# Performance work log

Hardware: AMD Instinct MI355X
Metric: run time of the kernel (lower is better)

The kernel has to match this reference:

```python
import jax, jax.numpy as jnp
import numpy as np

B, T, D, N, K, H = 2, 2048, 2048, 16, 8, 128
WIN = 1024                      # sliding_window_size
SOFT_CAP = 50.0                 # attn_logits_soft_cap
SCALAR = 0.08838834764831845    # query_pre_attn_scalar = head_dim**-0.5
K_MASK = -2.3819763e+38
ROPE_BASE = 10000.0
ROPE_SCALE = 1.0


def apply_rope(x, positions):
    # x: [B, T, heads, H]; positions: [B, T]
    head_dim = x.shape[-1]
    half = head_dim // 2
    timescale = ROPE_BASE ** (2.0 * jnp.arange(half, dtype=jnp.float32) / head_dim)
    sinusoid = positions[..., None].astype(jnp.float32) / timescale / ROPE_SCALE  # [B,T,half]
    sin = jnp.sin(sinusoid)[:, :, None, :]
    cos = jnp.cos(sinusoid)[:, :, None, :]
    first, second = jnp.split(x, 2, axis=-1)
    return jnp.concatenate(
        [first * cos - second * sin, second * cos + first * sin], axis=-1
    ).astype(x.dtype)


def setup_inputs() -> dict:
    key = jax.random.key(0)
    k0, k1, k2, k3 = jax.random.split(key, 4)
    x = jax.random.normal(k0, (B, T, D), jnp.float32)
    wq = jax.random.normal(k1, (N, D, H), jnp.float32) * (D ** -0.5)
    wkv = jax.random.normal(k2, (2, K, D, H), jnp.float32) * (D ** -0.5)
    wo = jax.random.normal(k3, (N, H, D), jnp.float32) * ((N * H) ** -0.5)
    segment_pos = jnp.broadcast_to(jnp.arange(T, dtype=jnp.int32), (B, T))
    attn_mask = jnp.broadcast_to(jnp.tril(jnp.ones((T, T), dtype=bool)), (B, T, T))  # causal
    return {"x": x, "wq": wq, "wkv": wkv, "wo": wo,
            "segment_pos": segment_pos, "attn_mask": attn_mask}


def reference(x, wq, wkv, wo, segment_pos, attn_mask):
    # --- projections ---
    q = jnp.einsum('BTD,NDH->BTNH', x, wq)          # [B,T,N,H]
    kv = jnp.einsum('BTD,CKDH->CBTKH', x, wkv)      # [2,B,T,K,H]
    k_proj, v_proj = kv[0], kv[1]
    # --- RoPE + query scaling ---
    q = apply_rope(q, segment_pos) * SCALAR
    k_proj = apply_rope(k_proj, segment_pos)
    # --- GQA logits ---
    G = N // K
    qg = q.reshape(B, T, K, G, H)
    logits = jnp.einsum('BTKGH,BSKH->BTKGS', qg, k_proj).reshape(B, T, N, T)
    # --- soft cap ---
    logits = jnp.tanh(logits / SOFT_CAP) * SOFT_CAP
    # --- sliding-window mask combined with causal attn_mask ---
    all_ones = jnp.ones(attn_mask.shape, dtype=attn_mask.dtype)
    sliding_mask = jnp.triu(all_ones, -WIN + 1) * jnp.tril(all_ones, WIN - 1)
    mask = sliding_mask * attn_mask                  # [B,T,S]
    padded_logits = jnp.where(mask[:, :, None, :], logits, K_MASK)
    probs = jax.nn.softmax(padded_logits, axis=-1).astype(k_proj.dtype)
    # --- GQA weighted values ---
    encoded = jnp.einsum('BTKGS,BSKH->BTKGH',
                         probs.reshape(B, T, K, G, T), v_proj).reshape(B, T, N, H)
    # --- output projection ---
    return jnp.einsum('BTNH,NHD->BTD', encoded, wo)
```

## Files before the change

### kernel.cpp

```cpp
#include <hip/hip_runtime.h>
#include <hip/hip_bf16.h>
#include <stdint.h>

#define BDIM 2
#define TDIM 2048
#define DDIM 2048
#define NHEADS 16
#define KVH 8
#define HDIM 128
#define WINSZ 1024
#define BT (BDIM*TDIM)
#define NHD (NHEADS*HDIM)
#define QKVC 4096

typedef unsigned short u16;
typedef __attribute__((ext_vector_type(8))) short bf16x8;
typedef __attribute__((ext_vector_type(4))) float f32x4;

__device__ __forceinline__ u16 f2bf(float f) {
  union { float f; unsigned u; } v; v.f = f;
  unsigned r = v.u + 0x7FFFu + ((v.u >> 16) & 1u);
  return (u16)(r >> 16);
}
__device__ __forceinline__ float bf2f(u16 u) {
  union { unsigned u; float f; } v; v.u = ((unsigned)u) << 16;
  return v.f;
}
__device__ __forceinline__ u16 cvt_bf(float f) {
  __hip_bfloat16 hb = __float2bfloat16(f);
  return *reinterpret_cast<u16*>(&hb);
}

__device__ __forceinline__ void gl_lds16(const u16* g, u16* l) {
  __builtin_amdgcn_global_load_lds((const __attribute__((address_space(1))) void*)g,
                                   (__attribute__((address_space(3))) void*)l, 16, 0, 0);
}

__global__ __launch_bounds__(256) void k_prep(const float* __restrict__ x, const float* __restrict__ wq,
                                              const float* __restrict__ wkv, const float* __restrict__ wo,
                                              const int* __restrict__ seg,
                                              u16* __restrict__ x_bf, u16* __restrict__ wt_qkv,
                                              u16* __restrict__ wo_t, float2* __restrict__ tab) {
  const int id = blockIdx.x, tid = threadIdx.x;
  if (id < 8192) {
    __shared__ float tl0[32][33];
    int tx = tid & 31, ty = tid >> 5;
    int r0 = (id & 127) * 32, c0 = (id >> 7) * 32;
    #pragma unroll
    for (int i = 0; i < 4; i++) {
      int r = r0 + tx, c = c0 + ty + i*8;
      const float* sp; size_t off;
      if (r < 2048) { sp = wq; off = (size_t)(r >> 7)*262144u + (size_t)(r & 127); }
      else { int j = r - 2048; sp = wkv; off = (size_t)((j >> 10)*8 + ((j >> 7) & 7))*262144u + (size_t)(j & 127); }
      off += (size_t)c * 128u;
      tl0[tx][ty + i*8] = sp[off];
    }
    __syncthreads();
    #pragma unroll
    for (int i = 0; i < 4; i++) {
      int rl = ty + i*8;
      wt_qkv[(size_t)(r0 + rl)*2048u + (size_t)(c0 + tx)] = f2bf(tl0[rl][tx]);
    }
  } else if (id < 16384) {
    int i = (id - 8192)*256 + tid;
    float4 v = ((const float4*)x)[i];
    ushort4 o;
    o.x = f2bf(v.x); o.y = f2bf(v.y); o.z = f2bf(v.z); o.w = f2bf(v.w);
    ((ushort4*)x_bf)[i] = o;
  } else if (id < 20480) {
    __shared__ float tl1[32][33];
    int id3 = id - 16384;
    int tx = tid & 31, ty = tid >> 5;
    int r0 = (id3 & 63) * 32, c0 = (id3 >> 6) * 32;
    #pragma unroll
    for (int i = 0; i < 4; i++) {
      int r = r0 + tx, c = c0 + ty + i*8;
      tl1[tx][ty + i*8] = wo[(size_t)c * 2048u + (size_t)r];
    }
    __syncthreads();
    #pragma unroll
    for (int i = 0; i < 4; i++) {
      int rl = ty + i*8;
      wo_t[(size_t)(r0 + rl)*2048u + (size_t)(c0 + tx)] = f2bf(tl1[rl][tx]);
    }
  } else {
    int bt = (id - 20480)*4 + (tid >> 6);
    int i = tid & 63;
    int pos = seg[bt];
    float inv_ts = exp2f(-(float)i * (13.287712379549449f/64.0f));
    float ang = (float)pos * inv_ts;
    tab[(size_t)bt*64 + i] = make_float2(cosf(ang), sinf(ang));
  }
}

template<int F32OUT>
__global__ __launch_bounds__(256) void k_gemm(const u16* __restrict__ A, const u16* __restrict__ Bt,
                                              void* __restrict__ Cout, int M, int Ncols, int Kdim, int ldc) {
  __shared__ u16 As[128*64];
  __shared__ u16 Bs[128*64];
  const int tid = threadIdx.x, lane = tid & 63, wave = tid >> 6;
  const int bid = blockIdx.x;
  const int xcd = bid & 7, idx = bid >> 3;
  const int m0 = (((xcd & 3) << 3) + (idx & 7)) * 128;
  const int n0 = (((xcd >> 2) << 3) + (idx >> 3)) * 128;
  const int wr = wave >> 1, wc = wave & 1;
  const int l15 = lane & 15, lg = lane >> 4;
  f32x4 acc[4][4] = {};
  for (int kt = 0; kt < Kdim; kt += 64) {
    __syncthreads();
    #pragma unroll
    for (int i = 0; i < 4; i++) {
      int chb = i*256 + wave*64;
      int ch = chb + lane;
      int r = ch >> 3, cc = ch & 7;
      gl_lds16(A + (size_t)(m0 + r)*Kdim + kt + cc*8, As + chb*8);
      gl_lds16(Bt + (size_t)(n0 + r)*Kdim + kt + cc*8, Bs + chb*8);
    }
    __syncthreads();
    #pragma unroll
    for (int ks = 0; ks < 2; ks++) {
      bf16x8 af[4], bf[4];
      int kk = ks*32 + lg*8;
      #pragma unroll
      for (int mt = 0; mt < 4; mt++) af[mt] = *(const bf16x8*)(As + (wr*64 + mt*16 + l15)*64 + kk);
      #pragma unroll
      for (int nt = 0; nt < 4; nt++) bf[nt] = *(const bf16x8*)(Bs + (wc*64 + nt*16 + l15)*64 + kk);
      #pragma unroll
      for (int mt = 0; mt < 4; mt++)
        #pragma unroll
        for (int nt = 0; nt < 4; nt++)
          acc[mt][nt] = __builtin_amdgcn_mfma_f32_16x16x32_bf16(af[mt], bf[nt], acc[mt][nt], 0, 0, 0);
    }
  }
  #pragma unroll
  for (int mt = 0; mt < 4; mt++) {
    int row = m0 + wr*64 + mt*16 + lg*4;
    #pragma unroll
    for (int nt = 0; nt < 4; nt++) {
      int col = n0 + wc*64 + nt*16 + l15;
      #pragma unroll
      for (int j = 0; j < 4; j++) {
        if (F32OUT) ((float*)Cout)[(size_t)(row + j)*ldc + col] = acc[mt][nt][j];
        else        ((u16*)Cout)[(size_t)(row + j)*ldc + col] = f2bf(acc[mt][nt][j]);
      }
    }
  }
}

__global__ __launch_bounds__(512, 2) void k_gemm8(const u16* __restrict__ A, const u16* __restrict__ Bt,
                                                  u16* __restrict__ Cout, u16* __restrict__ vT,
                                                  const float2* __restrict__ tab,
                                                  int M, int Ncols, int Kdim, int ldc) {
  __shared__ u16 As[2][256*64];
  __shared__ u16 Bs[2][256*64];
  const int tid = threadIdx.x, lane = tid & 63, wave = tid >> 6;
  const int l15 = lane & 15, lg = lane >> 4;
  const int wm = wave >> 2, wn = wave & 3;
  const int gx = M >> 8, gy = Ncols >> 8;
  const int nwg = gx * gy;
  int bid = blockIdx.x;
  int q = nwg >> 3, r = nwg & 7;
  int xcd = bid & 7, idx = bid >> 3;
  int wg = (xcd < r ? xcd*(q+1) : r*(q+1) + (xcd - r)*q) + idx;
  const int m0 = (wg % gx) * 256, n0 = (wg / gx) * 256;

  const int st_r = tid >> 3;
  const int st_c = (tid & 7) ^ (st_r & 7);

  const u16* Ag = A + (size_t)(m0 + st_r)*Kdim + st_c*8;
  const u16* Bg = Bt + (size_t)(n0 + st_r)*Kdim + st_c*8;

  auto stage = [&](int t, int h) {
    int buf = t & 1;
    if (h < 2) {
      const u16* g = Bg + (size_t)(h*128)*Kdim + t*64;
      u16* d = &Bs[buf][h*8192 + wave*512];
      gl_lds16(g, d);
      gl_lds16(g + (size_t)64*Kdim, d + 4096);
    } else {
      int hh = h - 2;
      const u16* g = Ag + (size_t)(hh*128)*Kdim + t*64;
      u16* d = &As[buf][hh*8192 + wave*512];
      gl_lds16(g, d);
      gl_lds16(g + (size_t)64*Kdim, d + 4096);
    }
  };

  const int aBase = (wm*128 + l15) * 128;
  const int bBase = (wn*16 + l15) * 128;
  const int kx0 = ((lg) ^ (l15 & 7)) << 4;
  const int kx1 = ((4 + lg) ^ (l15 & 7)) << 4;

  f32x4 acc[8][4] = {};
  bf16x8 af[4][2], bfr[4][2];

  stage(0,0); stage(0,1); stage(0,2); stage(0,3);
  asm volatile("s_waitcnt vmcnt(4)" ::: "memory");
  stage(1,0); stage(1,1); stage(1,2);
  asm volatile("s_waitcnt vmcnt(6)" ::: "memory");
  __builtin_amdgcn_s_barrier();

  const int NT = Kdim >> 6;

#define MFMA_Q(MS, NS)                                                          \
  { _Pragma("unroll") for (int mf = 0; mf < 4; mf++)                            \
    _Pragma("unroll") for (int nf = 0; nf < 2; nf++) {                          \
      acc[(MS)+mf][(NS)+nf] = __builtin_amdgcn_mfma_f32_16x16x32_bf16(af[mf][0], bfr[(NS)+nf][0], acc[(MS)+mf][(NS)+nf], 0, 0, 0); \
      acc[(MS)+mf][(NS)+nf] = __builtin_amdgcn_mfma_f32_16x16x32_bf16(af[mf][1], bfr[(NS)+nf][1], acc[(MS)+mf][(NS)+nf], 0, 0, 0); \
  } }

  for (int t = 0; t < NT; ++t) {
    const int cur = t & 1;
    const char* Ab = (const char*)&As[cur][0];
    const char* Bb = (const char*)&Bs[cur][0];
    #pragma unroll
    for (int mf = 0; mf < 4; mf++) {
      af[mf][0] = *(const bf16x8*)(Ab + aBase + mf*2048 + kx0);
      af[mf][1] = *(const bf16x8*)(Ab + aBase + mf*2048 + kx1);
    }
    #pragma unroll
    for (int nf = 0; nf < 2; nf++) {
      bfr[nf][0] = *(const bf16x8*)(Bb + bBase + nf*8192 + kx0);
      bfr[nf][1] = *(const bf16x8*)(Bb + bBase + nf*8192 + kx1);
    }
    if (t + 1 < NT) stage(t+1, 3);
    asm volatile("s_waitcnt lgkmcnt(8)" ::: "memory");
    __builtin_amdgcn_s_barrier();
    asm volatile("" ::: "memory");
    __builtin_amdgcn_s_setprio(1);
    MFMA_Q(0, 0)
    __builtin_amdgcn_s_setprio(0);
    __builtin_amdgcn_s_barrier();
    #pragma unroll
    for (int nf = 2; nf < 4; nf++) {
      bfr[nf][0] = *(const bf16x8*)(Bb + bBase + nf*8192 + kx0);
      bfr[nf][1] = *(const bf16x8*)(Bb + bBase + nf*8192 + kx1);
    }
    __builtin_amdgcn_s_barrier();
    asm volatile("" ::: "memory");
    __builtin_amdgcn_s_setprio(1);
    MFMA_Q(0, 2)
    __builtin_amdgcn_s_setprio(0);
    __builtin_amdgcn_s_barrier();
    #pragma unroll
    for (int mf = 0; mf < 4; mf++) {
      af[mf][0] = *(const bf16x8*)(Ab + aBase + 8192 + mf*2048 + kx0);
      af[mf][1] = *(const bf16x8*)(Ab + aBase + 8192 + mf*2048 + kx1);
    }
    if (t + 2 < NT) { stage(t+2, 0); stage(t+2, 1); }
    __builtin_amdgcn_s_barrier();
    asm volatile("" ::: "memory");
    __builtin_amdgcn_s_setprio(1);
    MFMA_Q(4, 2)
    __builtin_amdgcn_s_setprio(0);
    __builtin_amdgcn_s_barrier();
    if (t + 2 < NT) {
      stage(t+2, 2);
      asm volatile("s_waitcnt vmcnt(6)" ::: "memory");
    } else if (t + 1 < NT) {
      asm volatile("s_waitcnt vmcnt(0)" ::: "memory");
    }
    __builtin_amdgcn_s_barrier();
    asm volatile("" ::: "memory");
    __builtin_amdgcn_s_setprio(1);
    MFMA_Q(4, 0)
    __builtin_amdgcn_s_setprio(0);
    __builtin_amdgcn_s_barrier();
  }
#undef MFMA_Q

  const int type = (n0 < 2048) ? 0 : (n0 < 3072 ? 1 : 2);
  const float SC = 0.08838834764831845f;
  #pragma unroll
  for (int mf = 0; mf < 8; mf++) {
    int row = m0 + wm*128 + mf*16 + lg*4;
    if (type < 2) {
      #pragma unroll
      for (int j = 0; j < 4; j++) {
        float2 cs = tab[(size_t)(row + j)*64 + wn*16 + l15];
        #pragma unroll
        for (int pp = 0; pp < 4; pp += 2) {
          float f = acc[mf][pp][j], s = acc[mf][pp+1][j];
          float oa = f*cs.x - s*cs.y;
          float ob = s*cs.x + f*cs.y;
          if (type == 0) { oa *= SC; ob *= SC; }
          int col = n0 + pp*64 + wn*16 + l15;
          Cout[(size_t)(row + j)*ldc + col]      = cvt_bf(oa);
          Cout[(size_t)(row + j)*ldc + col + 64] = cvt_bf(ob);
        }
      }
    } else {
      int bb = row >> 11, tt = row & 2047;
      #pragma unroll
      for (int nf = 0; nf < 4; nf++) {
        int cb = n0 + nf*64 + wn*16 + l15 - 3072;
        int kvhh = cb >> 7, hh = cb & 127;
        ushort4 vv;
        vv.x = f2bf(acc[mf][nf][0]); vv.y = f2bf(acc[mf][nf][1]);
        vv.z = f2bf(acc[mf][nf][2]); vv.w = f2bf(acc[mf][nf][3]);
        *(ushort4*)(vT + ((size_t)(bb*KVH + kvhh)*HDIM + hh)*TDIM + tt) = vv;
      }
    }
  }
}

__device__ __forceinline__ void stage_tiles(const u16* __restrict__ kg, const u16* __restrict__ vg,
                                            u16* ldsK, u16* ldsV, int tid) {
  const int w = tid >> 6;
  const int rK = tid >> 4, cK = tid & 15;
  u16* dK = ldsK + w*512;
  gl_lds16(kg + (size_t)rK*QKVC + ((cK ^ (rK & 15)) << 3), dK);
  gl_lds16(kg + (size_t)(rK + 32)*QKVC + ((cK ^ ((rK + 32) & 15)) << 3), dK + 4096);
  const int rV = tid >> 3, cV = tid & 7;
  u16* dV = ldsV + w*512;
  gl_lds16(vg + (size_t)rV*TDIM + ((cV ^ (rV & 7)) << 3), dV);
  gl_lds16(vg + (size_t)(rV + 64)*TDIM + ((cV ^ ((rV + 64) & 7)) << 3), dV + 4096);
}

__global__ __launch_bounds__(512, 4) void k_attn(const u16* __restrict__ qkv, const u16* __restrict__ vT,
                                                 u16* __restrict__ enc) {
  __shared__ u16 Kb[2][64*128];
  __shared__ u16 Vb[2][128*64];
  __shared__ u16 Pl[8][16*32];
  const int tid = threadIdx.x;
  const int lane = tid & 63, wave = tid >> 6;
  const int l15 = lane & 15, lg = lane >> 4;
  const int wg = blockIdx.x;
  const int lin = (wg & 7)*64 + (wg >> 3);
  const int qt = lin & 31, kvh = (lin >> 5) & 7, b = lin >> 8;
  const int n = kvh*2 + (wave >> 2);
  const int t0 = qt * 64;
  const int lo_row = t0 + (wave & 3)*16, hi_row = lo_row + 15;

  bf16x8 qf[4];
  {
    const u16* qb = qkv + (size_t)(b*TDIM + lo_row + l15)*QKVC + n*HDIM + lg*8;
    #pragma unroll
    for (int ks = 0; ks < 4; ks++) qf[ks] = *(const bf16x8*)(qb + ks*32);
  }
  f32x4 o[8] = {};
  f32x4 o_l = {};
  const short one_bf = (short)0x3F80;
  const bf16x8 ones = {one_bf, one_bf, one_bf, one_bf, one_bf, one_bf, one_bf, one_bf};

  const u16* kgb = qkv + (size_t)(b*TDIM)*QKVC + 2048 + kvh*HDIM;
  const u16* vgb = vT + (size_t)(b*KVH + kvh)*HDIM*TDIM;

  const float L0 = 1.4426950408889634f;
  const float L1 = -1.9235933878519513e-4f;
  const float L2 = 3.0777094205631089e-8f;
  const float BIAS = -72.13475204444817f;

  const int s_begin = (t0 >= 1024) ? (t0 - 1024) : 0;
  stage_tiles(kgb + (size_t)s_begin*QKVC, vgb + s_begin, Kb[0], Vb[0], tid);
  int cur = 0;
  for (int s0 = s_begin; s0 <= t0; s0 += 64) {
    if (s0 + 64 <= t0) {
      stage_tiles(kgb + (size_t)(s0 + 64)*QKVC, vgb + (s0 + 64), Kb[cur ^ 1], Vb[cur ^ 1], tid);
      asm volatile("s_waitcnt vmcnt(4)" ::: "memory");
    } else {
      asm volatile("s_waitcnt vmcnt(0)" ::: "memory");
    }
    __builtin_amdgcn_s_barrier();
    __builtin_amdgcn_sched_barrier(0);

    const u16* Kc = Kb[cur];
    const u16* Vc = Vb[cur];
    f32x4 sc4[4];
    #pragma unroll
    for (int c = 0; c < 4; c++) {
      const int cLo = s0 + c*16;
      bool anyLive = (cLo <= hi_row) && (cLo + 15 >= lo_row - (WINSZ - 1));
      bool full    = (cLo + 15 <= lo_row) && (cLo >= hi_row - (WINSZ - 1));
      f32x4 a = {0.f, 0.f, 0.f, 0.f};
      if (anyLive) {
        int krow = c*16 + l15;
        __builtin_amdgcn_s_setprio(1);
        #pragma unroll
        for (int ks = 0; ks < 4; ks++) {
          bf16x8 kf = *(const bf16x8*)(Kc + krow*128 + (((ks*4 + lg) ^ l15) << 3));
          a = __builtin_amdgcn_mfma_f32_16x16x32_bf16(qf[ks], kf, a, 0, 0, 0);
        }
        __builtin_amdgcn_s_setprio(0);
        if (full) {
          #pragma unroll
          for (int j = 0; j < 4; j++) {
            float z = a[j];
            float u = z*z;
            float tt = __builtin_fmaf(u, __builtin_fmaf(u, L2, L1), L0);
            a[j] = exp2f(__builtin_fmaf(z, tt, BIAS));
          }
        } else {
          #pragma unroll
          for (int j = 0; j < 4; j++) {
            int scol = cLo + l15;
            int trow2 = lo_row + lg*4 + j;
            float z = a[j];
            float u = z*z;
            float tt = __builtin_fmaf(u, __builtin_fmaf(u, L2, L1), L0);
            float p = exp2f(__builtin_fmaf(z, tt, BIAS));
            bool ok = (scol <= trow2) && (scol >= trow2 - (WINSZ - 1));
            a[j] = ok ? p : 0.f;
          }
        }
      }
      sc4[c] = a;
    }
    __builtin_amdgcn_s_setprio(1);
    #pragma unroll
    for (int h = 0; h < 2; h++) {
      #pragma unroll
      for (int c2 = 0; c2 < 2; c2++) {
        int c = h*2 + c2;
        #pragma unroll
        for (int j = 0; j < 4; j++) {
          int prow = lg*4 + j, pcol = c2*16 + l15;
          int off = prow*64 + pcol*2; off ^= (prow & 3) << 4;
          *(u16*)((char*)(&Pl[wave][0]) + off) = cvt_bf(sc4[c][j]);
        }
      }
      int roff = l15*64 + ((lg ^ (l15 & 3)) << 4);
      bf16x8 pf = *(const bf16x8*)((char*)(&Pl[wave][0]) + roff);
      o_l = __builtin_amdgcn_mfma_f32_16x16x32_bf16(pf, ones, o_l, 0, 0, 0);
      #pragma unroll
      for (int ct = 0; ct < 8; ct++) {
        int vrow = ct*16 + l15;
        bf16x8 vf = *(const bf16x8*)(Vc + vrow*64 + (((h*4 + lg) ^ (l15 & 7)) << 3));
        o[ct] = __builtin_amdgcn_mfma_f32_16x16x32_bf16(pf, vf, o[ct], 0, 0, 0);
      }
      asm volatile("" ::: "memory");
    }
    __builtin_amdgcn_s_setprio(0);
    __builtin_amdgcn_s_barrier();
    cur ^= 1;
  }
  #pragma unroll
  for (int j = 0; j < 4; j++) {
    float inv = __fdividef(1.f, o_l[j]);
    int row = lo_row + lg*4 + j;
    u16* eb = enc + (size_t)(b*TDIM + row)*NHD + n*HDIM;
    #pragma unroll
    for (int ct = 0; ct < 8; ct++)
      eb[ct*16 + l15] = cvt_bf(o[ct][j] * inv);
  }
}

extern "C" void kernel_launch(void* const* d_in, const int* in_sizes, int n_in,
                              void* d_out, int out_size, void* d_ws, size_t ws_size,
                              hipStream_t stream) {
  const float* x   = (const float*)d_in[0];
  const float* wq  = (const float*)d_in[1];
  const float* wkv = (const float*)d_in[2];
  const float* wo  = (const float*)d_in[3];
  const int*   seg = (const int*)d_in[4];
  float* out = (float*)d_out;

  char* ws = (char*)d_ws;
  u16*    x_bf   = (u16*)(ws);
  u16*    wt_qkv = (u16*)(ws + (16u << 20));
  u16*    qkv    = (u16*)(ws + (32u << 20));
  u16*    vT     = (u16*)(ws + (64u << 20));
  u16*    enc    = (u16*)(ws + (72u << 20));
  u16*    wo_t   = (u16*)(ws + (88u << 20));
  float2* tab    = (float2*)(ws + (96u << 20));

  k_prep<<<dim3(21504), 256, 0, stream>>>(x, wq, wkv, wo, seg, x_bf, wt_qkv, wo_t, tab);
  k_gemm8<<<dim3((BT/256)*(QKVC/256)), 512, 0, stream>>>(x_bf, wt_qkv, qkv, vT, tab, BT, QKVC, DDIM, QKVC);
  k_attn<<<dim3(512), 512, 0, stream>>>(qkv, vT, enc);
  k_gemm<1><<<dim3(512), 256, 0, stream>>>(enc, wo_t, out, BT, DDIM, NHD, DDIM);
}
```

Before: 196.2 us.

## Give each attention wave two 16-row query tiles to reuse K/V fragments

The attention kernel drops from 8 to 4 waves per workgroup, and each wave now computes two 16-row query tiles. Each K and V fragment read from LDS feeds two MFMAs, which halves LDS read traffic per unit of MFMA work. Tile staging is redone for 256 threads with four loads each for K and V, and the wait count is adjusted to match. The cost is roughly twice the accumulator registers per wave and fewer waves to hide latency, with launch bounds changed to 256 threads and 2 blocks.

```diff
diff --git a/kernel.cpp b/kernel.cpp
--- a/kernel.cpp
+++ b/kernel.cpp
@@ -306,40 +306,46 @@
 
 __device__ __forceinline__ void stage_tiles(const u16* __restrict__ kg, const u16* __restrict__ vg,
                                             u16* ldsK, u16* ldsV, int tid) {
-  const int w = tid >> 6;
-  const int rK = tid >> 4, cK = tid & 15;
-  u16* dK = ldsK + w*512;
-  gl_lds16(kg + (size_t)rK*QKVC + ((cK ^ (rK & 15)) << 3), dK);
-  gl_lds16(kg + (size_t)(rK + 32)*QKVC + ((cK ^ ((rK + 32) & 15)) << 3), dK + 4096);
-  const int rV = tid >> 3, cV = tid & 7;
-  u16* dV = ldsV + w*512;
-  gl_lds16(vg + (size_t)rV*TDIM + ((cV ^ (rV & 7)) << 3), dV);
-  gl_lds16(vg + (size_t)(rV + 64)*TDIM + ((cV ^ ((rV + 64) & 7)) << 3), dV + 4096);
-}
-
-__global__ __launch_bounds__(512, 4) void k_attn(const u16* __restrict__ qkv, const u16* __restrict__ vT,
+  const int w4 = (tid >> 6) * 4;
+  #pragma unroll
+  for (int i = 0; i < 4; i++) {
+    int ri = w4 + i;
+    int rK = ri*4 + ((tid >> 4) & 3);
+    int cK = (tid & 15) ^ (rK & 15);
+    gl_lds16(kg + (size_t)rK*QKVC + (cK << 3), ldsK + ri*512);
+    int rV = ri*8 + ((tid >> 3) & 7);
+    int cV = (tid & 7) ^ (rV & 7);
+    gl_lds16(vg + (size_t)rV*TDIM + (cV << 3), ldsV + ri*512);
+  }
+}
+
+__global__ __launch_bounds__(256, 2) void k_attn(const u16* __restrict__ qkv, const u16* __restrict__ vT,
                                                  u16* __restrict__ enc) {
   __shared__ u16 Kb[2][64*128];
   __shared__ u16 Vb[2][128*64];
-  __shared__ u16 Pl[8][16*32];
+  __shared__ u16 Pl[4][32*32];
   const int tid = threadIdx.x;
   const int lane = tid & 63, wave = tid >> 6;
   const int l15 = lane & 15, lg = lane >> 4;
   const int wg = blockIdx.x;
   const int lin = (wg & 7)*64 + (wg >> 3);
   const int qt = lin & 31, kvh = (lin >> 5) & 7, b = lin >> 8;
-  const int n = kvh*2 + (wave >> 2);
+  const int n = kvh*2 + (wave >> 1);
   const int t0 = qt * 64;
-  const int lo_row = t0 + (wave & 3)*16, hi_row = lo_row + 15;
-
-  bf16x8 qf[4];
+  const int lo = t0 + (wave & 1)*32;
+
+  bf16x8 qf0[4], qf1[4];
   {
-    const u16* qb = qkv + (size_t)(b*TDIM + lo_row + l15)*QKVC + n*HDIM + lg*8;
-    #pragma unroll
-    for (int ks = 0; ks < 4; ks++) qf[ks] = *(const bf16x8*)(qb + ks*32);
-  }
-  f32x4 o[8] = {};
-  f32x4 o_l = {};
+    const u16* qb0 = qkv + (size_t)(b*TDIM + lo + l15)*QKVC + n*HDIM + lg*8;
+    const u16* qb1 = qb0 + (size_t)16*QKVC;
+    #pragma unroll
+    for (int ks = 0; ks < 4; ks++) {
+      qf0[ks] = *(const bf16x8*)(qb0 + ks*32);
+      qf1[ks] = *(const bf16x8*)(qb1 + ks*32);
+    }
+  }
+  f32x4 o0[8] = {}, o1[8] = {};
+  f32x4 ol0 = {}, ol1 = {};
   const short one_bf = (short)0x3F80;
   const bf16x8 ones = {one_bf, one_bf, one_bf, one_bf, one_bf, one_bf, one_bf, one_bf};
 
@@ -350,6 +356,24 @@
   const float L1 = -1.9235933878519513e-4f;
   const float L2 = 3.0777094205631089e-8f;
   const float BIAS = -72.13475204444817f;
+
+  auto smx = [&](f32x4 a, bool full, int rowb, int cLo) -> f32x4 {
+    #pragma unroll
+    for (int j = 0; j < 4; j++) {
+      float z = a[j];
+      float u = z*z;
+      float tt = __builtin_fmaf(u, __builtin_fmaf(u, L2, L1), L0);
+      float p = exp2f(__builtin_fmaf(z, tt, BIAS));
+      if (!full) {
+        int scol = cLo + l15;
+        int trow = rowb + lg*4 + j;
+        bool ok = (scol <= trow) && (scol >= trow - (WINSZ - 1));
+        p = ok ? p : 0.f;
+      }
+      a[j] = p;
+    }
+    return a;
+  };
 
   const int s_begin = (t0 >= 1024) ? (t0 - 1024) : 0;
   stage_tiles(kgb + (size_t)s_begin*QKVC, vgb + s_begin, Kb[0], Vb[0], tid);
@@ -357,7 +381,7 @@
   for (int s0 = s_begin; s0 <= t0; s0 += 64) {
     if (s0 + 64 <= t0) {
       stage_tiles(kgb + (size_t)(s0 + 64)*QKVC, vgb + (s0 + 64), Kb[cur ^ 1], Vb[cur ^ 1], tid);
-      asm volatile("s_waitcnt vmcnt(4)" ::: "memory");
+      asm volatile("s_waitcnt vmcnt(8)" ::: "memory");
     } else {
       asm volatile("s_waitcnt vmcnt(0)" ::: "memory");
     }
@@ -366,45 +390,30 @@
 
     const u16* Kc = Kb[cur];
     const u16* Vc = Vb[cur];
-    f32x4 sc4[4];
+    f32x4 s0f[4], s1f[4];
     #pragma unroll
     for (int c = 0; c < 4; c++) {
       const int cLo = s0 + c*16;
-      bool anyLive = (cLo <= hi_row) && (cLo + 15 >= lo_row - (WINSZ - 1));
-      bool full    = (cLo + 15 <= lo_row) && (cLo >= hi_row - (WINSZ - 1));
-      f32x4 a = {0.f, 0.f, 0.f, 0.f};
-      if (anyLive) {
+      const bool live0 = (cLo <= lo + 15) && (cLo + 15 >= lo - (WINSZ - 1));
+      const bool live1 = (cLo <= lo + 31) && (cLo + 15 >= lo + 16 - (WINSZ - 1));
+      const bool full0 = (cLo + 15 <= lo) && (cLo >= lo + 15 - (WINSZ - 1));
+      const bool full1 = (cLo + 15 <= lo + 16) && (cLo >= lo + 31 - (WINSZ - 1));
+      f32x4 a0 = {0.f, 0.f, 0.f, 0.f}, a1 = {0.f, 0.f, 0.f, 0.f};
+      if (live0 || live1) {
         int krow = c*16 + l15;
         __builtin_amdgcn_s_setprio(1);
         #pragma unroll
         for (int ks = 0; ks < 4; ks++) {
           bf16x8 kf = *(const bf16x8*)(Kc + krow*128 + (((ks*4 + lg) ^ l15) << 3));
-          a = __builtin_amdgcn_mfma_f32_16x16x32_bf16(qf[ks], kf, a, 0, 0, 0);
+          a0 = __builtin_amdgcn_mfma_f32_16x16x32_bf16(qf0[ks], kf, a0, 0, 0, 0);
+          a1 = __builtin_amdgcn_mfma_f32_16x16x32_bf16(qf1[ks], kf, a1, 0, 0, 0);
         }
         __builtin_amdgcn_s_setprio(0);
-        if (full) {
-          #pragma unroll
-          for (int j = 0; j < 4; j++) {
-            float z = a[j];
-            float u = z*z;
-            float tt = __builtin_fmaf(u, __builtin_fmaf(u, L2, L1), L0);
-            a[j] = exp2f(__builtin_fmaf(z, tt, BIAS));
-          }
-        } else {
-          #pragma unroll
-          for (int j = 0; j < 4; j++) {
-            int scol = cLo + l15;
-            int trow2 = lo_row + lg*4 + j;
-            float z = a[j];
-            float u = z*z;
-            float tt = __builtin_fmaf(u, __builtin_fmaf(u, L2, L1), L0);
-            float p = exp2f(__builtin_fmaf(z, tt, BIAS));
-            bool ok = (scol <= trow2) && (scol >= trow2 - (WINSZ - 1));
-            a[j] = ok ? p : 0.f;
-          }
-        }
-      }
-      sc4[c] = a;
+      }
+      if (live0) s0f[c] = smx(a0, full0, lo, cLo);
+      else       s0f[c] = (f32x4){0.f, 0.f, 0.f, 0.f};
+      if (live1) s1f[c] = smx(a1, full1, lo + 16, cLo);
+      else       s1f[c] = (f32x4){0.f, 0.f, 0.f, 0.f};
     }
     __builtin_amdgcn_s_setprio(1);
     #pragma unroll
@@ -414,19 +423,26 @@
         int c = h*2 + c2;
         #pragma unroll
         for (int j = 0; j < 4; j++) {
-          int prow = lg*4 + j, pcol = c2*16 + l15;
-          int off = prow*64 + pcol*2; off ^= (prow & 3) << 4;
-          *(u16*)((char*)(&Pl[wave][0]) + off) = cvt_bf(sc4[c][j]);
+          int pr0 = lg*4 + j, pc = c2*16 + l15;
+          int off0 = pr0*64 + pc*2; off0 ^= (pr0 & 3) << 4;
+          *(u16*)((char*)(&Pl[wave][0]) + off0) = cvt_bf(s0f[c][j]);
+          int pr1 = 16 + lg*4 + j;
+          int off1 = pr1*64 + pc*2; off1 ^= (pr1 & 3) << 4;
+          *(u16*)((char*)(&Pl[wave][0]) + off1) = cvt_bf(s1f[c][j]);
         }
       }
-      int roff = l15*64 + ((lg ^ (l15 & 3)) << 4);
-      bf16x8 pf = *(const bf16x8*)((char*)(&Pl[wave][0]) + roff);
-      o_l = __builtin_amdgcn_mfma_f32_16x16x32_bf16(pf, ones, o_l, 0, 0, 0);
+      int r0off = l15*64 + ((lg ^ (l15 & 3)) << 4);
+      int r1off = (16 + l15)*64 + ((lg ^ (l15 & 3)) << 4);
+      bf16x8 pf0 = *(const bf16x8*)((char*)(&Pl[wave][0]) + r0off);
+      bf16x8 pf1 = *(const bf16x8*)((char*)(&Pl[wave][0]) + r1off);
+      ol0 = __builtin_amdgcn_mfma_f32_16x16x32_bf16(pf0, ones, ol0, 0, 0, 0);
+      ol1 = __builtin_amdgcn_mfma_f32_16x16x32_bf16(pf1, ones, ol1, 0, 0, 0);
       #pragma unroll
       for (int ct = 0; ct < 8; ct++) {
         int vrow = ct*16 + l15;
         bf16x8 vf = *(const bf16x8*)(Vc + vrow*64 + (((h*4 + lg) ^ (l15 & 7)) << 3));
-        o[ct] = __builtin_amdgcn_mfma_f32_16x16x32_bf16(pf, vf, o[ct], 0, 0, 0);
+        o0[ct] = __builtin_amdgcn_mfma_f32_16x16x32_bf16(pf0, vf, o0[ct], 0, 0, 0);
+        o1[ct] = __builtin_amdgcn_mfma_f32_16x16x32_bf16(pf1, vf, o1[ct], 0, 0, 0);
       }
       asm volatile("" ::: "memory");
     }
@@ -436,12 +452,16 @@
   }
   #pragma unroll
   for (int j = 0; j < 4; j++) {
-    float inv = __fdividef(1.f, o_l[j]);
-    int row = lo_row + lg*4 + j;
-    u16* eb = enc + (size_t)(b*TDIM + row)*NHD + n*HDIM;
-    #pragma unroll
-    for (int ct = 0; ct < 8; ct++)
-      eb[ct*16 + l15] = cvt_bf(o[ct][j] * inv);
+    float inv0 = __fdividef(1.f, ol0[j]);
+    float inv1 = __fdividef(1.f, ol1[j]);
+    int row0 = lo + lg*4 + j;
+    u16* eb0 = enc + (size_t)(b*TDIM + row0)*NHD + n*HDIM;
+    u16* eb1 = eb0 + (size_t)16*NHD;
+    #pragma unroll
+    for (int ct = 0; ct < 8; ct++) {
+      eb0[ct*16 + l15] = cvt_bf(o0[ct][j] * inv0);
+      eb1[ct*16 + l15] = cvt_bf(o1[ct][j] * inv1);
+    }
   }
 }
 
@@ -466,6 +486,6 @@
 
   k_prep<<<dim3(21504), 256, 0, stream>>>(x, wq, wkv, wo, seg, x_bf, wt_qkv, wo_t, tab);
   k_gemm8<<<dim3((BT/256)*(QKVC/256)), 512, 0, stream>>>(x_bf, wt_qkv, qkv, vT, tab, BT, QKVC, DDIM, QKVC);
-  k_attn<<<dim3(512), 512, 0, stream>>>(qkv, vT, enc);
+  k_attn<<<dim3(512), 256, 0, stream>>>(qkv, vT, enc);
   k_gemm<1><<<dim3(512), 256, 0, stream>>>(enc, wo_t, out, BT, DDIM, NHD, DDIM);
 }
```

Result: slower. 211.0 us (+7.6%).
